# Optimization experiments

Hardware: AMD Instinct MI355X
Metric: run time of the kernel (lower is better)

The kernel has to match this reference:

```python
import jax, jax.numpy as jnp
import numpy as np

# dims
B, TQ, NQ, DQ = 2, 32, 196, 896      # batch, chunks, queries/chunk, slow-feat dim
T, H, W, CIN = 32, 8, 8, 4           # fast feature video dims
EMB = 1024                           # fast input mapping (kv) dim
HID = 512                            # cross_attn_hidden_dim
NH = 4                               # heads
HD = HID // NH                       # head dim = 128
HALF = HD // 2                       # 64 rotary freq channels
SEC = [22, 21, 21]                   # 3D rope sections (t,h,w) over the 64 freqs
FF = 2 * HID
OUT = 896
BASE = 10000.0
QGRID = 14                           # 196 = 14x14 query spatial grid
EPS = 1e-5


def _p(key, shape, scale=0.02):
    return (jax.random.normal(key, shape, dtype=jnp.float32) * scale)


def setup_inputs() -> dict:
    key = jax.random.key(0)
    ks = jax.random.split(key, 20)
    inp = {
        "x": jax.random.normal(ks[0], (B, T, H, W, CIN), dtype=jnp.float32),
        "slow_feats": jax.random.normal(ks[1], (B, TQ, NQ, DQ), dtype=jnp.float32),
        "frame_num": jnp.full((B,), T, dtype=jnp.int32),
        # query_input_mapping: 896 -> 512
        "Wq_in": _p(ks[2], (DQ, HID)), "bq_in": jnp.zeros((HID,), jnp.float32),
        # fast input_mapping (linear): 4 -> 1024
        "Wm": _p(ks[3], (CIN, EMB)), "bm": jnp.zeros((EMB,), jnp.float32),
        # cross-attn projections
        "Wq": _p(ks[4], (HID, HID)), "bq": jnp.zeros((HID,), jnp.float32),
        "Wk": _p(ks[5], (EMB, HID)), "bk": jnp.zeros((HID,), jnp.float32),
        "Wv": _p(ks[6], (EMB, HID)), "bv": jnp.zeros((HID,), jnp.float32),
        "Wo": _p(ks[7], (HID, HID)), "bo": jnp.zeros((HID,), jnp.float32),
        # decoder layer norms + FFN (dim_feedforward = 2*hidden)
        "g1": jnp.ones((HID,), jnp.float32), "be1": jnp.zeros((HID,), jnp.float32),
        "W1": _p(ks[8], (HID, FF)), "b1": jnp.zeros((FF,), jnp.float32),
        "W2": _p(ks[9], (FF, HID)), "b2": jnp.zeros((HID,), jnp.float32),
        "g2": jnp.ones((HID,), jnp.float32), "be2": jnp.zeros((HID,), jnp.float32),
        # output MLP (mlp_depth=2): 512 -> 1024 -> GELU -> 896
        "M1": _p(ks[10], (HID, 2 * HID)), "bm1": jnp.zeros((2 * HID,), jnp.float32),
        "M2": _p(ks[11], (2 * HID, OUT)), "bm2": jnp.zeros((OUT,), jnp.float32),
    }
    return inp


def _ln(x, g, b):
    m = x.mean(-1, keepdims=True)
    v = jnp.var(x, axis=-1, keepdims=True)
    return (x - m) * jax.lax.rsqrt(v + EPS) * g + b


def _rope_cos_sin(pos):
    # pos: (N,3) float (t,h,w). Qwen2-style inv_freq over head_dim=128.
    inv_freq = 1.0 / (BASE ** (jnp.arange(0, HD, 2, dtype=jnp.float32) / HD))  # (64,)
    sel = jnp.asarray([0] * SEC[0] + [1] * SEC[1] + [2] * SEC[2])              # (64,)
    freqs = pos[:, sel] * inv_freq                                             # (N,64)
    emb = jnp.concatenate([freqs, freqs], axis=-1)                             # (N,128)
    return jnp.cos(emb), jnp.sin(emb)


def _rot_half(x):
    return jnp.concatenate([-x[..., HALF:], x[..., :HALF]], axis=-1)


def _positions():
    # query tokens: (chunk t, 14x14 grid)
    qt = jnp.repeat(jnp.arange(TQ), NQ)
    qg = jnp.tile(jnp.arange(NQ), TQ)
    q_pos = jnp.stack([qt, qg // QGRID, qg % QGRID], axis=-1).astype(jnp.float32)  # (6272,3)
    # kv tokens: (frame t, HxW grid)
    kt = jnp.repeat(jnp.arange(T), H * W)
    kg = jnp.tile(jnp.arange(H * W), T)
    k_pos = jnp.stack([kt, kg // W, kg % W], axis=-1).astype(jnp.float32)          # (2048,3)
    return q_pos, k_pos


def _forward(x, slow_feats, Wq_in, bq_in, Wm, bm, Wq, bq, Wk, bk, Wv, bv,
             Wo, bo, g1, be1, W1, b1, W2, b2, g2, be2, M1, bm1, M2, bm2):
    q_pos, k_pos = _positions()
    cos_q, sin_q = _rope_cos_sin(q_pos)   # (Nq,128)
    cos_k, sin_k = _rope_cos_sin(k_pos)   # (Nk,128)
    scale = 1.0 / jnp.sqrt(jnp.float32(HD))

    def per_sample(xi, si):
        # slow feats -> queries: (32,196,896) -> (6272,512)
        q_in = (si.reshape(TQ * NQ, DQ) @ Wq_in + bq_in)
        # fast feats -> kv tokens: (T,H,W,Cin) -> (2048,1024)
        kv = (xi.reshape(T * H * W, CIN) @ Wm + bm)
        # projections -> heads
        q = (q_in @ Wq + bq).reshape(-1, NH, HD)
        k = (kv @ Wk + bk).reshape(-1, NH, HD)
        v = (kv @ Wv + bv).reshape(-1, NH, HD)
        # 3D RoPE on q and k
        q = q * cos_q[:, None, :] + _rot_half(q) * sin_q[:, None, :]
        k = k * cos_k[:, None, :] + _rot_half(k) * sin_k[:, None, :]
        # cross attention
        attn = jnp.einsum('qhd,khd->hqk', q, k) * scale
        attn = jax.nn.softmax(attn, axis=-1)
        o = jnp.einsum('hqk,khd->qhd', attn, v).reshape(-1, HID)
        o = o @ Wo + bo
        # residual + norm + FFN + norm (post-norm decoder layer)
        h = _ln(q_in + o, g1, be1)
        ff = jax.nn.gelu(h @ W1 + b1) @ W2 + b2
        h = _ln(h + ff, g2, be2)
        # output MLP: Linear -> GELU -> Linear
        y = jax.nn.gelu(h @ M1 + bm1) @ M2 + bm2
        return y  # (6272, 896)

    return jax.vmap(per_sample)(x, slow_feats)  # (B, 6272, 896)


def reference(x, slow_feats, frame_num, Wq_in, bq_in, Wm, bm, Wq, bq, Wk, bk,
              Wv, bv, Wo, bo, g1, be1, W1, b1, W2, b2, g2, be2, M1, bm1, M2, bm2):
    # frame_num is the valid-frame count per sample; here all samples are full
    # length (frame_num == T), so no KV masking is needed.
    del frame_num
    return _forward(x, slow_feats, Wq_in, bq_in, Wm, bm, Wq, bq, Wk, bk, Wv, bv,
                    Wo, bo, g1, be1, W1, b1, W2, b2, g2, be2, M1, bm1, M2, bm2)
```

## Files before the change

kernel.cpp:

```cpp
#include <hip/hip_runtime.h>
#include <cstdint>
#include <cstddef>

#define BATCH 2
#define MQ 12544
#define ROWS_Q 6272
#define MK 4096
#define ROWS_K 2048
#define HID 512
#define NH 4
#define HD 128
#define EMB 1024
#define DQ 896
#define FF 1024
#define OUTD 896

typedef __bf16 bf16;
typedef unsigned int u32;
typedef bf16 bf16x8 __attribute__((ext_vector_type(8)));
typedef float f32x4 __attribute__((ext_vector_type(4)));

enum { OP_BIAS = 0, OP_GELU = 1, OP_RES = 2 };

__device__ __forceinline__ float gelu_tanh(float x) {
    float x3 = x * x * x;
    return 0.5f * x * (1.0f + tanhf(0.7978845608028654f * (x + 0.044715f * x3)));
}

__device__ __forceinline__ void gld16(const bf16* g, bf16* l) {
    __builtin_amdgcn_global_load_lds(
        (const __attribute__((address_space(1))) unsigned int*)g,
        (__attribute__((address_space(3))) unsigned int*)l, 16, 0, 0);
}

__device__ __forceinline__ u32 pack_bf16(float a, float b) {
    union { bf16 h[2]; u32 w; } u;
    u.h[0] = (bf16)a; u.h[1] = (bf16)b;
    return u.w;
}

template <int OP, bool WF32, bool WB16>
__global__ __launch_bounds__(256) void mgemm(
    const bf16* __restrict__ A, const bf16* __restrict__ Bt,
    const float* __restrict__ bias, const float* __restrict__ res,
    float* __restrict__ Cf, bf16* __restrict__ Cb, int M, int N, int K)
{
    __shared__ __align__(16) bf16 As[128 * 32];
    __shared__ __align__(16) bf16 Bs[128 * 32];
    const int tid  = threadIdx.x;
    const int m0   = blockIdx.y * 128;
    const int n0   = blockIdx.x * 128;
    const int wave = tid >> 6, lane = tid & 63;
    const int wm = (wave >> 1) * 64, wn = (wave & 1) * 64;

    f32x4 acc[4][4] = {};

    const int srow = tid >> 2;
    const int scol = (tid & 3) * 8;
    const bf16* Ag = A  + (size_t)(m0 + srow) * K + scol;
    const bf16* Bg = Bt + (size_t)(n0 + srow) * K + scol;
    bf16* Al = &As[tid * 8];
    bf16* Bl = &Bs[tid * 8];
    const size_t half = (size_t)64 * K;

    const int fr = lane & 15;
    const int kq = (lane >> 4) * 8;
    const bf16* pa = &As[(wm + fr) * 32 + kq];
    const bf16* pb = &Bs[(wn + fr) * 32 + kq];

    for (int k0 = 0; k0 < K; k0 += 32) {
        gld16(Ag + k0,        Al);
        gld16(Ag + k0 + half, Al + 64 * 32);
        gld16(Bg + k0,        Bl);
        gld16(Bg + k0 + half, Bl + 64 * 32);
        __syncthreads();

        bf16x8 af[4], bfr[4];
        #pragma unroll
        for (int i = 0; i < 4; ++i) af[i]  = *(const bf16x8*)(pa + i * 16 * 32);
        #pragma unroll
        for (int j = 0; j < 4; ++j) bfr[j] = *(const bf16x8*)(pb + j * 16 * 32);
        #pragma unroll
        for (int i = 0; i < 4; ++i)
            #pragma unroll
            for (int j = 0; j < 4; ++j)
                acc[i][j] = __builtin_amdgcn_mfma_f32_16x16x32_bf16(
                    af[i], bfr[j], acc[i][j], 0, 0, 0);
        __syncthreads();
    }

    const int colb = n0 + wn + (lane & 15);
    const int rowb = m0 + wm + (lane >> 4) * 4;
    #pragma unroll
    for (int i = 0; i < 4; ++i) {
        #pragma unroll
        for (int j = 0; j < 4; ++j) {
            const int c = colb + j * 16;
            const float bj = bias[c];
            #pragma unroll
            for (int r = 0; r < 4; ++r) {
                const int m = rowb + i * 16 + r;
                float v = acc[i][j][r] + bj;
                if (OP == OP_GELU) v = gelu_tanh(v);
                if (OP == OP_RES)  v += res[(size_t)m * N + c];
                if (WF32) Cf[(size_t)m * N + c] = v;
                if (WB16) Cb[(size_t)m * N + c] = (bf16)v;
            }
        }
    }
}

__global__ __launch_bounds__(256) void transpose_kernel(
    const float* __restrict__ W, bf16* __restrict__ Wt, int K, int N)
{
    __shared__ float t[32][33];
    const int bx = blockIdx.x;
    const int by = blockIdx.y;
    const int x = threadIdx.x & 31, y = threadIdx.x >> 5;
    #pragma unroll
    for (int i = 0; i < 32; i += 8)
        t[y + i][x] = W[(size_t)(by * 32 + y + i) * N + bx * 32 + x];
    __syncthreads();
    #pragma unroll
    for (int i = 0; i < 32; i += 8)
        Wt[(size_t)(bx * 32 + y + i) * K + by * 32 + x] = (bf16)t[x][y + i];
}

__global__ __launch_bounds__(256) void cvt_kernel(
    const float* __restrict__ in, bf16* __restrict__ out, int n4)
{
    int i = blockIdx.x * 256 + threadIdx.x;
    if (i >= n4) return;
    float4 v = ((const float4*)in)[i];
    out[4 * i + 0] = (bf16)v.x;
    out[4 * i + 1] = (bf16)v.y;
    out[4 * i + 2] = (bf16)v.z;
    out[4 * i + 3] = (bf16)v.w;
}

__global__ __launch_bounds__(256) void kv_kernel(
    const float* __restrict__ x, const float* __restrict__ Wm,
    const float* __restrict__ bm, bf16* __restrict__ kv)
{
    int idx = blockIdx.x * 256 + threadIdx.x;
    int r = idx >> 10, n = idx & 1023;
    float4 xv = *(const float4*)(x + (size_t)r * 4);
    float v = bm[n] + xv.x * Wm[n] + xv.y * Wm[1024 + n]
                    + xv.z * Wm[2048 + n] + xv.w * Wm[3072 + n];
    kv[idx] = (bf16)v;
}

__global__ __launch_bounds__(256) void rope_b_kernel(
    const bf16* __restrict__ in, bf16* __restrict__ out,
    int tok, int gdiv, int wdiv, int total, float sc)
{
    int idx = blockIdx.x * 256 + threadIdx.x;
    if (idx >= total) return;
    int row = idx >> 7;
    int r2 = idx & 127;
    int h = r2 >> 5;
    int j2 = r2 & 31;
    int j = 2 * j2;
    int n = row % tok;
    int t = n / gdiv;
    int g = n % gdiv;
    int gh = g / wdiv;
    int gw = g % wdiv;
    float pa = (j < 22) ? (float)t : (j < 43) ? (float)gh : (float)gw;
    int j1 = j + 1;
    float pb = (j1 < 22) ? (float)t : (j1 < 43) ? (float)gh : (float)gw;
    float fra = pa * exp2f(-(float)j  * 0.20762050593045954f);
    float frb = pb * exp2f(-(float)j1 * 0.20762050593045954f);
    float ca = cosf(fra), sa = sinf(fra);
    float cb = cosf(frb), sb = sinf(frb);
    size_t base = (size_t)row * 512 + (size_t)h * 128 + j;
    union { u32 w; bf16 e[2]; } ua, ub;
    ua.w = *(const u32*)(in + base);
    ub.w = *(const u32*)(in + base + 64);
    float x1a = (float)ua.e[0], x1b = (float)ua.e[1];
    float x2a = (float)ub.e[0], x2b = (float)ub.e[1];
    *(u32*)(out + base)      = pack_bf16((x1a * ca - x2a * sa) * sc,
                                         (x1b * cb - x2b * sb) * sc);
    *(u32*)(out + base + 64) = pack_bf16((x2a * ca + x1a * sa) * sc,
                                         (x2b * cb + x1b * sb) * sc);
}

__global__ __launch_bounds__(256) void vt_kernel(
    const bf16* __restrict__ v16, bf16* __restrict__ vt)
{
    int idx = blockIdx.x * 256 + threadIdx.x;
    int t = idx & 2047;
    int d = (idx >> 11) & 127;
    int bh = idx >> 18;
    int b = bh >> 2, h = bh & 3;
    vt[idx] = v16[(size_t)(b * ROWS_K + t) * HID + h * HD + d];
}

__global__ __launch_bounds__(256) void ln_kernel(
    float* __restrict__ xb, const float* __restrict__ g,
    const float* __restrict__ be, bf16* __restrict__ out16)
{
    int wave = threadIdx.x >> 6, lane = threadIdx.x & 63;
    size_t row = (size_t)blockIdx.x * 4 + wave;
    float* xp = xb + row * 512;
    float4 a = ((const float4*)xp)[lane];
    float4 b = ((const float4*)xp)[lane + 64];
    float s  = a.x + a.y + a.z + a.w + b.x + b.y + b.z + b.w;
    float sq = a.x*a.x + a.y*a.y + a.z*a.z + a.w*a.w
             + b.x*b.x + b.y*b.y + b.z*b.z + b.w*b.w;
    #pragma unroll
    for (int off = 32; off; off >>= 1) {
        s  += __shfl_xor(s, off);
        sq += __shfl_xor(sq, off);
    }
    float mean = s * (1.0f / 512.0f);
    float var  = sq * (1.0f / 512.0f) - mean * mean;
    float rstd = rsqrtf(var + 1e-5f);
    float4 gv1 = ((const float4*)g)[lane],  gv2 = ((const float4*)g)[lane + 64];
    float4 bv1 = ((const float4*)be)[lane], bv2 = ((const float4*)be)[lane + 64];
    a.x = (a.x - mean) * rstd * gv1.x + bv1.x;
    a.y = (a.y - mean) * rstd * gv1.y + bv1.y;
    a.z = (a.z - mean) * rstd * gv1.z + bv1.z;
    a.w = (a.w - mean) * rstd * gv1.w + bv1.w;
    b.x = (b.x - mean) * rstd * gv2.x + bv2.x;
    b.y = (b.y - mean) * rstd * gv2.y + bv2.y;
    b.z = (b.z - mean) * rstd * gv2.z + bv2.z;
    b.w = (b.w - mean) * rstd * gv2.w + bv2.w;
    ((float4*)xp)[lane]      = a;
    ((float4*)xp)[lane + 64] = b;
    bf16* op = out16 + row * 512;
    *(u32*)(op + lane * 4)       = pack_bf16(a.x, a.y);
    *(u32*)(op + lane * 4 + 2)   = pack_bf16(a.z, a.w);
    *(u32*)(op + 256 + lane * 4)     = pack_bf16(b.x, b.y);
    *(u32*)(op + 256 + lane * 4 + 2) = pack_bf16(b.z, b.w);
}

__global__ __launch_bounds__(256, 2) void mattn_kernel(
    const bf16* __restrict__ qs, const bf16* __restrict__ ks,
    const bf16* __restrict__ vt, bf16* __restrict__ outb)
{
    __shared__ __align__(16) char smem[35840];
    bf16* Ksh = (bf16*)smem;
    bf16* Vsh = (bf16*)(smem + 17408);

    const int tid = threadIdx.x;
    const int wave = tid >> 6, lane = tid & 63;
    const int quad = lane >> 4, c = lane & 15;
    const int bid = blockIdx.x;
    const int qt = bid % 49;
    const int h  = (bid / 49) & 3;
    const int b  = bid / 196;

    const int q0 = qt * 128 + wave * 32;
    const bf16* qg = qs + (size_t)(b * ROWS_Q + q0) * HID + h * HD;
    const bf16* kg = ks + (size_t)(b * ROWS_K) * HID + h * HD;
    const bf16* vg = vt + (size_t)(b * NH + h) * HD * ROWS_K;

    bf16x8 qf[2][4];
    #pragma unroll
    for (int n = 0; n < 2; ++n)
        #pragma unroll
        for (int s = 0; s < 4; ++s)
            qf[n][s] = *(const bf16x8*)(qg + (size_t)(n * 16 + c) * HID + s * 32 + quad * 8);

    f32x4 o[8][2] = {};
    float m_i[2] = {-1e30f, -1e30f}, l_i[2] = {0.0f, 0.0f};

    const int st_t = tid >> 2;
    const int st_d = (tid & 3) * 32;
    const int sv_d = tid >> 1;
    const int sv_t = (tid & 1) * 32;

    for (int kt = 0; kt < 32; ++kt) {
        __syncthreads();
        {
            const bf16* src = kg + (size_t)(kt * 64 + st_t) * HID + st_d;
            bf16* dst = Ksh + st_t * 136 + st_d;
            #pragma unroll
            for (int i = 0; i < 4; ++i)
                *(bf16x8*)(dst + i * 8) = *(const bf16x8*)(src + i * 8);
        }
        {
            const bf16* src = vg + (size_t)sv_d * ROWS_K + kt * 64 + sv_t;
            bf16* dst = Vsh + sv_d * 72 + sv_t;
            #pragma unroll
            for (int i = 0; i < 4; ++i)
                *(bf16x8*)(dst + i * 8) = *(const bf16x8*)(src + i * 8);
        }
        __syncthreads();

        f32x4 s[4][2] = {};
        #pragma unroll
        for (int ksi = 0; ksi < 4; ++ksi) {
            bf16x8 kf[4];
            #pragma unroll
            for (int mi = 0; mi < 4; ++mi)
                kf[mi] = *(const bf16x8*)(Ksh + (mi * 16 + c) * 136 + ksi * 32 + quad * 8);
            #pragma unroll
            for (int mi = 0; mi < 4; ++mi)
                #pragma unroll
                for (int n = 0; n < 2; ++n)
                    s[mi][n] = __builtin_amdgcn_mfma_f32_16x16x32_bf16(
                        kf[mi], qf[n][ksi], s[mi][n], 0, 0, 0);
        }

        float alpha[2];
        #pragma unroll
        for (int n = 0; n < 2; ++n) {
            float mx = -1e30f;
            #pragma unroll
            for (int mi = 0; mi < 4; ++mi)
                #pragma unroll
                for (int r = 0; r < 4; ++r) mx = fmaxf(mx, s[mi][n][r]);
            mx = fmaxf(mx, __shfl_xor(mx, 16));
            mx = fmaxf(mx, __shfl_xor(mx, 32));
            float mn = fmaxf(m_i[n], mx);
            alpha[n] = __expf(m_i[n] - mn);
            m_i[n] = mn;
            float sm = 0.0f;
            #pragma unroll
            for (int mi = 0; mi < 4; ++mi)
                #pragma unroll
                for (int r = 0; r < 4; ++r) {
                    float p = __expf(s[mi][n][r] - mn);
                    s[mi][n][r] = p;
                    sm += p;
                }
            sm += __shfl_xor(sm, 16);
            sm += __shfl_xor(sm, 32);
            l_i[n] = l_i[n] * alpha[n] + sm;
            #pragma unroll
            for (int md = 0; md < 8; ++md) {
                o[md][n][0] *= alpha[n]; o[md][n][1] *= alpha[n];
                o[md][n][2] *= alpha[n]; o[md][n][3] *= alpha[n];
            }
        }

        u32 pk[4][2][2];
        #pragma unroll
        for (int mi = 0; mi < 4; ++mi)
            #pragma unroll
            for (int n = 0; n < 2; ++n) {
                pk[mi][n][0] = pack_bf16(s[mi][n][0], s[mi][n][1]);
                pk[mi][n][1] = pack_bf16(s[mi][n][2], s[mi][n][3]);
            }
        bf16x8 pf[2][2];
        #pragma unroll
        for (int kst = 0; kst < 2; ++kst)
            #pragma unroll
            for (int n = 0; n < 2; ++n) {
                union { bf16x8 v8; u32 d[4]; } u;
                #pragma unroll
                for (int dw = 0; dw < 4; ++dw) {
                    int srcl = ((quad & 1) * 2 + (dw >> 1)) * 16 + c;
                    u32 lo = (u32)__shfl((int)pk[2 * kst][n][dw & 1], srcl);
                    u32 hi = (u32)__shfl((int)pk[2 * kst + 1][n][dw & 1], srcl);
                    u.d[dw] = (quad >= 2) ? hi : lo;
                }
                pf[kst][n] = u.v8;
            }

        #pragma unroll
        for (int kst = 0; kst < 2; ++kst)
            #pragma unroll
            for (int md = 0; md < 8; ++md) {
                bf16x8 vf = *(const bf16x8*)(Vsh + (md * 16 + c) * 72 + kst * 32 + quad * 8);
                #pragma unroll
                for (int n = 0; n < 2; ++n)
                    o[md][n] = __builtin_amdgcn_mfma_f32_16x16x32_bf16(
                        vf, pf[kst][n], o[md][n], 0, 0, 0);
            }
    }

    __syncthreads();
    bf16* Osh = (bf16*)smem + wave * (32 * 136);
    float inv[2] = {1.0f / l_i[0], 1.0f / l_i[1]};
    #pragma unroll
    for (int md = 0; md < 8; ++md)
        #pragma unroll
        for (int n = 0; n < 2; ++n)
            #pragma unroll
            for (int hh = 0; hh < 2; ++hh) {
                u32 w = pack_bf16(o[md][n][2 * hh] * inv[n], o[md][n][2 * hh + 1] * inv[n]);
                int d = md * 16 + quad * 4 + 2 * hh;
                int qq = n * 16 + c;
                *(u32*)(Osh + qq * 136 + d) = w;
            }
    __syncthreads();
    bf16* og = outb + (size_t)(b * ROWS_Q + q0) * HID + h * HD;
    #pragma unroll
    for (int i = 0; i < 8; ++i) {
        int idx = i * 64 + lane;
        int qq = idx >> 4;
        int ch = idx & 15;
        bf16x8 vv = *(const bf16x8*)(Osh + qq * 136 + ch * 8);
        *(bf16x8*)(og + (size_t)qq * HID + ch * 8) = vv;
    }
}

extern "C" void kernel_launch(void* const* d_in, const int* in_sizes, int n_in,
                              void* d_out, int out_size, void* d_ws, size_t ws_size,
                              hipStream_t stream)
{
    const float* x     = (const float*)d_in[0];
    const float* slow  = (const float*)d_in[1];
    const float* Wq_in = (const float*)d_in[3];
    const float* bq_in = (const float*)d_in[4];
    const float* Wm    = (const float*)d_in[5];
    const float* bm    = (const float*)d_in[6];
    const float* Wq    = (const float*)d_in[7];
    const float* bq    = (const float*)d_in[8];
    const float* Wk    = (const float*)d_in[9];
    const float* bk    = (const float*)d_in[10];
    const float* Wv    = (const float*)d_in[11];
    const float* bv    = (const float*)d_in[12];
    const float* Wo    = (const float*)d_in[13];
    const float* bo    = (const float*)d_in[14];
    const float* g1    = (const float*)d_in[15];
    const float* be1   = (const float*)d_in[16];
    const float* W1    = (const float*)d_in[17];
    const float* b1    = (const float*)d_in[18];
    const float* W2    = (const float*)d_in[19];
    const float* b2    = (const float*)d_in[20];
    const float* g2    = (const float*)d_in[21];
    const float* be2   = (const float*)d_in[22];
    const float* M1    = (const float*)d_in[23];
    const float* bm1   = (const float*)d_in[24];
    const float* M2    = (const float*)d_in[25];
    const float* bm2   = (const float*)d_in[26];
    float* out = (float*)d_out;

    float* q_in_f = (float*)d_ws;
    float* ob     = q_in_f + (size_t)MQ * HID;
    bf16* shared_b = (bf16*)(ob + (size_t)MQ * HID);
    bf16* q_in_b = shared_b + (size_t)MQ * FF;
    bf16* kv_b   = q_in_b + (size_t)MQ * HID;
    bf16* h_b    = kv_b + (size_t)MK * EMB;
    bf16* q16    = h_b + (size_t)MQ * HID;
    bf16* k16    = q16 + (size_t)MQ * HID;
    bf16* v16    = k16 + (size_t)MK * HID;
    bf16* qbt    = v16 + (size_t)MK * HID;
    bf16* kbt    = qbt + (size_t)MQ * HID;
    bf16* Vt     = kbt + (size_t)MK * HID;
    bf16* Wq_in_t = Vt + (size_t)8 * HD * ROWS_K;
    bf16* Wq_t = Wq_in_t + 512 * 896;
    bf16* Wk_t = Wq_t + 512 * 512;
    bf16* Wv_t = Wk_t + 512 * 1024;
    bf16* Wo_t = Wv_t + 512 * 1024;
    bf16* W1_t = Wo_t + 512 * 512;
    bf16* W2_t = W1_t + 1024 * 512;
    bf16* M1_t = W2_t + 512 * 1024;
    bf16* M2_t = M1_t + 1024 * 512;
    bf16* slow_b = shared_b;
    bf16* attn_b = shared_b;
    bf16* ff1_b  = shared_b;
    bf16* m1_b   = shared_b;

    dim3 blk(256);

    transpose_kernel<<<dim3(512 / 32, 896 / 32),  blk, 0, stream>>>(Wq_in, Wq_in_t, 896, 512);
    transpose_kernel<<<dim3(512 / 32, 512 / 32),  blk, 0, stream>>>(Wq, Wq_t, 512, 512);
    transpose_kernel<<<dim3(512 / 32, 1024 / 32), blk, 0, stream>>>(Wk, Wk_t, 1024, 512);
    transpose_kernel<<<dim3(512 / 32, 1024 / 32), blk, 0, stream>>>(Wv, Wv_t, 1024, 512);
    transpose_kernel<<<dim3(512 / 32, 512 / 32),  blk, 0, stream>>>(Wo, Wo_t, 512, 512);
    transpose_kernel<<<dim3(1024 / 32, 512 / 32), blk, 0, stream>>>(W1, W1_t, 512, 1024);
    transpose_kernel<<<dim3(512 / 32, 1024 / 32), blk, 0, stream>>>(W2, W2_t, 1024, 512);
    transpose_kernel<<<dim3(1024 / 32, 512 / 32), blk, 0, stream>>>(M1, M1_t, 512, 1024);
    transpose_kernel<<<dim3(896 / 32, 1024 / 32), blk, 0, stream>>>(M2, M2_t, 1024, 896);

    cvt_kernel<<<(MQ * DQ / 4 + 255) / 256, blk, 0, stream>>>(slow, slow_b, MQ * DQ / 4);
    kv_kernel<<<(MK * EMB) / 256, blk, 0, stream>>>(x, Wm, bm, kv_b);

    mgemm<OP_BIAS, true, true><<<dim3(4, 98), blk, 0, stream>>>(
        slow_b, Wq_in_t, bq_in, nullptr, q_in_f, q_in_b, MQ, HID, DQ);
    mgemm<OP_BIAS, false, true><<<dim3(4, 98), blk, 0, stream>>>(
        q_in_b, Wq_t, bq, nullptr, nullptr, q16, MQ, HID, HID);
    mgemm<OP_BIAS, false, true><<<dim3(4, 32), blk, 0, stream>>>(
        kv_b, Wk_t, bk, nullptr, nullptr, k16, MK, HID, EMB);
    mgemm<OP_BIAS, false, true><<<dim3(4, 32), blk, 0, stream>>>(
        kv_b, Wv_t, bv, nullptr, nullptr, v16, MK, HID, EMB);
    rope_b_kernel<<<(MQ * 128 + 255) / 256, blk, 0, stream>>>(
        q16, qbt, ROWS_Q, 196, 14, MQ * 128, 0.08838834764831843f);
    rope_b_kernel<<<(MK * 128 + 255) / 256, blk, 0, stream>>>(
        k16, kbt, ROWS_K, 64, 8, MK * 128, 1.0f);
    vt_kernel<<<(8 * HD * ROWS_K) / 256, blk, 0, stream>>>(v16, Vt);
    mattn_kernel<<<dim3(392), blk, 0, stream>>>(qbt, kbt, Vt, attn_b);
    mgemm<OP_RES, true, false><<<dim3(4, 98), blk, 0, stream>>>(
        attn_b, Wo_t, bo, q_in_f, ob, nullptr, MQ, HID, HID);
    ln_kernel<<<MQ / 4, blk, 0, stream>>>(ob, g1, be1, h_b);
    mgemm<OP_GELU, false, true><<<dim3(8, 98), blk, 0, stream>>>(
        h_b, W1_t, b1, nullptr, nullptr, ff1_b, MQ, FF, HID);
    mgemm<OP_RES, true, false><<<dim3(4, 98), blk, 0, stream>>>(
        ff1_b, W2_t, b2, ob, q_in_f, nullptr, MQ, HID, FF);
    ln_kernel<<<MQ / 4, blk, 0, stream>>>(q_in_f, g2, be2, h_b);
    mgemm<OP_GELU, false, true><<<dim3(8, 98), blk, 0, stream>>>(
        h_b, M1_t, bm1, nullptr, nullptr, m1_b, MQ, 2 * HID, HID);
    mgemm<OP_BIAS, true, false><<<dim3(7, 98), blk, 0, stream>>>(
        m1_b, M2_t, bm2, nullptr, out, nullptr, MQ, OUTD, 2 * HID);
}
```

Before: 617.0 us.

## Add 64-row GEMM tile, fuse K/V projections, batch transposes, tile V transpose

Adds a 64x128-tile GEMM variant, used for the N=512 GEMMs so they launch twice as many blocks and fill the GPU's compute units better. Fuses the K and V projections into one GEMM with concatenated weights and bias. Merges the nine weight-transpose launches into a single kernel. Replaces the scalar V transpose with an LDS-tiled version. Smaller tiles give less data reuse per block, and the two extra memcpy calls add some launch overhead.

Result: faster. 579.9 us (-6.0%).

```diff
diff --git a/kernel.cpp b/kernel.cpp
--- a/kernel.cpp
+++ b/kernel.cpp
@@ -18,6 +18,7 @@
 typedef __bf16 bf16;
 typedef unsigned int u32;
 typedef bf16 bf16x8 __attribute__((ext_vector_type(8)));
+typedef bf16 bf16x4 __attribute__((ext_vector_type(4)));
 typedef float f32x4 __attribute__((ext_vector_type(4)));
 
 enum { OP_BIAS = 0, OP_GELU = 1, OP_RES = 2 };
@@ -110,20 +111,100 @@
     }
 }
 
-__global__ __launch_bounds__(256) void transpose_kernel(
-    const float* __restrict__ W, bf16* __restrict__ Wt, int K, int N)
+template <int OP, bool WF32, bool WB16>
+__global__ __launch_bounds__(256) void mgemm64(
+    const bf16* __restrict__ A, const bf16* __restrict__ Bt,
+    const float* __restrict__ bias, const float* __restrict__ res,
+    float* __restrict__ Cf, bf16* __restrict__ Cb, int M, int N, int K)
+{
+    __shared__ __align__(16) bf16 As[64 * 32];
+    __shared__ __align__(16) bf16 Bs[128 * 32];
+    const int tid  = threadIdx.x;
+    const int m0   = blockIdx.y * 64;
+    const int n0   = blockIdx.x * 128;
+    const int wave = tid >> 6, lane = tid & 63;
+    const int wm = (wave >> 1) * 32, wn = (wave & 1) * 64;
+
+    f32x4 acc[2][4] = {};
+
+    const int srow = tid >> 2;
+    const int scol = (tid & 3) * 8;
+    const bf16* Ag = A  + (size_t)(m0 + srow) * K + scol;
+    const bf16* Bg = Bt + (size_t)(n0 + srow) * K + scol;
+    bf16* Al = &As[tid * 8];
+    bf16* Bl = &Bs[tid * 8];
+    const size_t half = (size_t)64 * K;
+
+    const int fr = lane & 15;
+    const int kq = (lane >> 4) * 8;
+    const bf16* pa = &As[(wm + fr) * 32 + kq];
+    const bf16* pb = &Bs[(wn + fr) * 32 + kq];
+
+    for (int k0 = 0; k0 < K; k0 += 32) {
+        gld16(Ag + k0,        Al);
+        gld16(Bg + k0,        Bl);
+        gld16(Bg + k0 + half, Bl + 64 * 32);
+        __syncthreads();
+
+        bf16x8 af[2], bfr[4];
+        #pragma unroll
+        for (int i = 0; i < 2; ++i) af[i]  = *(const bf16x8*)(pa + i * 16 * 32);
+        #pragma unroll
+        for (int j = 0; j < 4; ++j) bfr[j] = *(const bf16x8*)(pb + j * 16 * 32);
+        #pragma unroll
+        for (int i = 0; i < 2; ++i)
+            #pragma unroll
+            for (int j = 0; j < 4; ++j)
+                acc[i][j] = __builtin_amdgcn_mfma_f32_16x16x32_bf16(
+                    af[i], bfr[j], acc[i][j], 0, 0, 0);
+        __syncthreads();
+    }
+
+    const int colb = n0 + wn + (lane & 15);
+    const int rowb = m0 + wm + (lane >> 4) * 4;
+    #pragma unroll
+    for (int i = 0; i < 2; ++i) {
+        #pragma unroll
+        for (int j = 0; j < 4; ++j) {
+            const int c = colb + j * 16;
+            const float bj = bias[c];
+            #pragma unroll
+            for (int r = 0; r < 4; ++r) {
+                const int m = rowb + i * 16 + r;
+                float v = acc[i][j][r] + bj;
+                if (OP == OP_GELU) v = gelu_tanh(v);
+                if (OP == OP_RES)  v += res[(size_t)m * N + c];
+                if (WF32) Cf[(size_t)m * N + c] = v;
+                if (WB16) Cb[(size_t)m * N + c] = (bf16)v;
+            }
+        }
+    }
+}
+
+struct TDesc { const float* src; bf16* dst; int K; int N; int tile0; };
+struct TDescs { TDesc d[9]; };
+
+__global__ __launch_bounds__(256) void transpose_all(TDescs td)
 {
     __shared__ float t[32][33];
-    const int bx = blockIdx.x;
-    const int by = blockIdx.y;
+    const int blk = blockIdx.x;
+    int i = 0;
+    #pragma unroll
+    for (int j = 1; j < 9; ++j) if (blk >= td.d[j].tile0) i = j;
+    const float* src = td.d[i].src;
+    bf16* dst = td.d[i].dst;
+    const int K = td.d[i].K, N = td.d[i].N;
+    const int local = blk - td.d[i].tile0;
+    const int ntx = N >> 5;
+    const int bx = local % ntx, by = local / ntx;
     const int x = threadIdx.x & 31, y = threadIdx.x >> 5;
     #pragma unroll
-    for (int i = 0; i < 32; i += 8)
-        t[y + i][x] = W[(size_t)(by * 32 + y + i) * N + bx * 32 + x];
+    for (int p = 0; p < 32; p += 8)
+        t[y + p][x] = src[(size_t)(by * 32 + y + p) * N + bx * 32 + x];
     __syncthreads();
     #pragma unroll
-    for (int i = 0; i < 32; i += 8)
-        Wt[(size_t)(bx * 32 + y + i) * K + by * 32 + x] = (bf16)t[x][y + i];
+    for (int p = 0; p < 32; p += 8)
+        dst[(size_t)(bx * 32 + y + p) * K + by * 32 + x] = (bf16)t[x][y + p];
 }
 
 __global__ __launch_bounds__(256) void cvt_kernel(
@@ -152,7 +233,7 @@
 
 __global__ __launch_bounds__(256) void rope_b_kernel(
     const bf16* __restrict__ in, bf16* __restrict__ out,
-    int tok, int gdiv, int wdiv, int total, float sc)
+    int tok, int gdiv, int wdiv, int total, float sc, int istr, int icoff)
 {
     int idx = blockIdx.x * 256 + threadIdx.x;
     if (idx >= total) return;
@@ -173,27 +254,44 @@
     float frb = pb * exp2f(-(float)j1 * 0.20762050593045954f);
     float ca = cosf(fra), sa = sinf(fra);
     float cb = cosf(frb), sb = sinf(frb);
-    size_t base = (size_t)row * 512 + (size_t)h * 128 + j;
+    size_t ibase = (size_t)row * istr + icoff + (size_t)h * 128 + j;
+    size_t obase = (size_t)row * 512 + (size_t)h * 128 + j;
     union { u32 w; bf16 e[2]; } ua, ub;
-    ua.w = *(const u32*)(in + base);
-    ub.w = *(const u32*)(in + base + 64);
+    ua.w = *(const u32*)(in + ibase);
+    ub.w = *(const u32*)(in + ibase + 64);
     float x1a = (float)ua.e[0], x1b = (float)ua.e[1];
     float x2a = (float)ub.e[0], x2b = (float)ub.e[1];
-    *(u32*)(out + base)      = pack_bf16((x1a * ca - x2a * sa) * sc,
-                                         (x1b * cb - x2b * sb) * sc);
-    *(u32*)(out + base + 64) = pack_bf16((x2a * ca + x1a * sa) * sc,
-                                         (x2b * cb + x1b * sb) * sc);
-}
-
-__global__ __launch_bounds__(256) void vt_kernel(
-    const bf16* __restrict__ v16, bf16* __restrict__ vt)
-{
-    int idx = blockIdx.x * 256 + threadIdx.x;
-    int t = idx & 2047;
-    int d = (idx >> 11) & 127;
-    int bh = idx >> 18;
-    int b = bh >> 2, h = bh & 3;
-    vt[idx] = v16[(size_t)(b * ROWS_K + t) * HID + h * HD + d];
+    *(u32*)(out + obase)      = pack_bf16((x1a * ca - x2a * sa) * sc,
+                                          (x1b * cb - x2b * sb) * sc);
+    *(u32*)(out + obase + 64) = pack_bf16((x2a * ca + x1a * sa) * sc,
+                                          (x2b * cb + x1b * sb) * sc);
+}
+
+__global__ __launch_bounds__(256) void vt_tiled(
+    const bf16* __restrict__ kv16, bf16* __restrict__ vt)
+{
+    __shared__ bf16 t[64][72];
+    const int tt = blockIdx.x * 64;
+    const int d0 = blockIdx.y * 64;
+    const int bh = blockIdx.z;
+    const int b = bh >> 2, h = bh & 3;
+    const int rr = threadIdx.x >> 4;
+    const int cc = (threadIdx.x & 15) * 4;
+    #pragma unroll
+    for (int p = 0; p < 4; ++p) {
+        int r = rr + p * 16;
+        *(bf16x4*)&t[r][cc] = *(const bf16x4*)
+            (kv16 + (size_t)(b * ROWS_K + tt + r) * 1024 + 512 + h * 128 + d0 + cc);
+    }
+    __syncthreads();
+    #pragma unroll
+    for (int p = 0; p < 4; ++p) {
+        int r = rr + p * 16;
+        bf16x4 v;
+        v[0] = t[cc + 0][r]; v[1] = t[cc + 1][r];
+        v[2] = t[cc + 2][r]; v[3] = t[cc + 3][r];
+        *(bf16x4*)(vt + (size_t)bh * HD * ROWS_K + (size_t)(d0 + r) * ROWS_K + tt + cc) = v;
+    }
 }
 
 __global__ __launch_bounds__(256) void ln_kernel(
@@ -432,25 +530,24 @@
 
     float* q_in_f = (float*)d_ws;
     float* ob     = q_in_f + (size_t)MQ * HID;
-    bf16* shared_b = (bf16*)(ob + (size_t)MQ * HID);
+    float* bkv    = ob + (size_t)MQ * HID;
+    bf16* shared_b = (bf16*)(bkv + 1024);
     bf16* q_in_b = shared_b + (size_t)MQ * FF;
     bf16* kv_b   = q_in_b + (size_t)MQ * HID;
     bf16* h_b    = kv_b + (size_t)MK * EMB;
     bf16* q16    = h_b + (size_t)MQ * HID;
-    bf16* k16    = q16 + (size_t)MQ * HID;
-    bf16* v16    = k16 + (size_t)MK * HID;
-    bf16* qbt    = v16 + (size_t)MK * HID;
+    bf16* kv16   = q16 + (size_t)MQ * HID;
+    bf16* qbt    = kv16 + (size_t)MK * EMB;
     bf16* kbt    = qbt + (size_t)MQ * HID;
     bf16* Vt     = kbt + (size_t)MK * HID;
     bf16* Wq_in_t = Vt + (size_t)8 * HD * ROWS_K;
-    bf16* Wq_t = Wq_in_t + 512 * 896;
-    bf16* Wk_t = Wq_t + 512 * 512;
-    bf16* Wv_t = Wk_t + 512 * 1024;
-    bf16* Wo_t = Wv_t + 512 * 1024;
-    bf16* W1_t = Wo_t + 512 * 512;
-    bf16* W2_t = W1_t + 1024 * 512;
-    bf16* M1_t = W2_t + 512 * 1024;
-    bf16* M2_t = M1_t + 1024 * 512;
+    bf16* Wq_t  = Wq_in_t + 512 * 896;
+    bf16* kvw_t = Wq_t + 512 * 512;
+    bf16* Wo_t  = kvw_t + 1024 * 1024;
+    bf16* W1_t  = Wo_t + 512 * 512;
+    bf16* W2_t  = W1_t + 1024 * 512;
+    bf16* M1_t  = W2_t + 512 * 1024;
+    bf16* M2_t  = M1_t + 1024 * 512;
     bf16* slow_b = shared_b;
     bf16* attn_b = shared_b;
     bf16* ff1_b  = shared_b;
@@ -458,39 +555,47 @@
 
     dim3 blk(256);
 
-    transpose_kernel<<<dim3(512 / 32, 896 / 32),  blk, 0, stream>>>(Wq_in, Wq_in_t, 896, 512);
-    transpose_kernel<<<dim3(512 / 32, 512 / 32),  blk, 0, stream>>>(Wq, Wq_t, 512, 512);
-    transpose_kernel<<<dim3(512 / 32, 1024 / 32), blk, 0, stream>>>(Wk, Wk_t, 1024, 512);
-    transpose_kernel<<<dim3(512 / 32, 1024 / 32), blk, 0, stream>>>(Wv, Wv_t, 1024, 512);
-    transpose_kernel<<<dim3(512 / 32, 512 / 32),  blk, 0, stream>>>(Wo, Wo_t, 512, 512);
-    transpose_kernel<<<dim3(1024 / 32, 512 / 32), blk, 0, stream>>>(W1, W1_t, 512, 1024);
-    transpose_kernel<<<dim3(512 / 32, 1024 / 32), blk, 0, stream>>>(W2, W2_t, 1024, 512);
-    transpose_kernel<<<dim3(1024 / 32, 512 / 32), blk, 0, stream>>>(M1, M1_t, 512, 1024);
-    transpose_kernel<<<dim3(896 / 32, 1024 / 32), blk, 0, stream>>>(M2, M2_t, 1024, 896);
+    TDescs td;
+    int t0 = 0;
+    auto set = [&](int i, const float* s, bf16* d, int K, int N) {
+        td.d[i] = {s, d, K, N, t0};
+        t0 += (N / 32) * (K / 32);
+    };
+    set(0, Wq_in, Wq_in_t, 896, 512);
+    set(1, Wq,    Wq_t,    512, 512);
+    set(2, Wk,    kvw_t,              1024, 512);
+    set(3, Wv,    kvw_t + 512 * 1024, 1024, 512);
+    set(4, Wo,    Wo_t,    512, 512);
+    set(5, W1,    W1_t,    512, 1024);
+    set(6, W2,    W2_t,    1024, 512);
+    set(7, M1,    M1_t,    512, 1024);
+    set(8, M2,    M2_t,    1024, 896);
+    transpose_all<<<t0, blk, 0, stream>>>(td);
+
+    hipMemcpyAsync(bkv,       bk, 512 * sizeof(float), hipMemcpyDeviceToDevice, stream);
+    hipMemcpyAsync(bkv + 512, bv, 512 * sizeof(float), hipMemcpyDeviceToDevice, stream);
 
     cvt_kernel<<<(MQ * DQ / 4 + 255) / 256, blk, 0, stream>>>(slow, slow_b, MQ * DQ / 4);
     kv_kernel<<<(MK * EMB) / 256, blk, 0, stream>>>(x, Wm, bm, kv_b);
 
-    mgemm<OP_BIAS, true, true><<<dim3(4, 98), blk, 0, stream>>>(
+    mgemm64<OP_BIAS, true, true><<<dim3(4, 196), blk, 0, stream>>>(
         slow_b, Wq_in_t, bq_in, nullptr, q_in_f, q_in_b, MQ, HID, DQ);
-    mgemm<OP_BIAS, false, true><<<dim3(4, 98), blk, 0, stream>>>(
+    mgemm64<OP_BIAS, false, true><<<dim3(4, 196), blk, 0, stream>>>(
         q_in_b, Wq_t, bq, nullptr, nullptr, q16, MQ, HID, HID);
-    mgemm<OP_BIAS, false, true><<<dim3(4, 32), blk, 0, stream>>>(
-        kv_b, Wk_t, bk, nullptr, nullptr, k16, MK, HID, EMB);
-    mgemm<OP_BIAS, false, true><<<dim3(4, 32), blk, 0, stream>>>(
-        kv_b, Wv_t, bv, nullptr, nullptr, v16, MK, HID, EMB);
+    mgemm64<OP_BIAS, false, true><<<dim3(8, 64), blk, 0, stream>>>(
+        kv_b, kvw_t, bkv, nullptr, nullptr, kv16, MK, 1024, EMB);
     rope_b_kernel<<<(MQ * 128 + 255) / 256, blk, 0, stream>>>(
-        q16, qbt, ROWS_Q, 196, 14, MQ * 128, 0.08838834764831843f);
+        q16, qbt, ROWS_Q, 196, 14, MQ * 128, 0.08838834764831843f, 512, 0);
     rope_b_kernel<<<(MK * 128 + 255) / 256, blk, 0, stream>>>(
-        k16, kbt, ROWS_K, 64, 8, MK * 128, 1.0f);
-    vt_kernel<<<(8 * HD * ROWS_K) / 256, blk, 0, stream>>>(v16, Vt);
+        kv16, kbt, ROWS_K, 64, 8, MK * 128, 1.0f, 1024, 0);
+    vt_tiled<<<dim3(32, 2, 8), blk, 0, stream>>>(kv16, Vt);
     mattn_kernel<<<dim3(392), blk, 0, stream>>>(qbt, kbt, Vt, attn_b);
-    mgemm<OP_RES, true, false><<<dim3(4, 98), blk, 0, stream>>>(
+    mgemm64<OP_RES, true, false><<<dim3(4, 196), blk, 0, stream>>>(
         attn_b, Wo_t, bo, q_in_f, ob, nullptr, MQ, HID, HID);
     ln_kernel<<<MQ / 4, blk, 0, stream>>>(ob, g1, be1, h_b);
     mgemm<OP_GELU, false, true><<<dim3(8, 98), blk, 0, stream>>>(
         h_b, W1_t, b1, nullptr, nullptr, ff1_b, MQ, FF, HID);
-    mgemm<OP_RES, true, false><<<dim3(4, 98), blk, 0, stream>>>(
+    mgemm64<OP_RES, true, false><<<dim3(4, 196), blk, 0, stream>>>(
         ff1_b, W2_t, b2, ob, q_in_f, nullptr, MQ, HID, FF);
     ln_kernel<<<MQ / 4, blk, 0, stream>>>(q_in_f, g2, be2, h_b);
     mgemm<OP_GELU, false, true><<<dim3(8, 98), blk, 0, stream>>>(
```
